# Performance work log

Measured on AMD Instinct MI355X. Metric: run time of the kernel, lower is better.

## Reference

```python
import jax, jax.numpy as jnp
import numpy as np

N = 4096          # number of real POIs (distance_matrix is [N, N])
D = 64            # poi_dim
B = 8             # users (samples)
DAYS = 4          # days per user
L = 64            # POI ids per day
SCALE = 50.0      # max distance -> arange(0, 50+0.5, 0.5) = 101 bucket boundaries
NUM_INTERVALS = 101


def setup_inputs() -> dict:
    key = jax.random.key(0)
    k1, k2, k3 = jax.random.split(key, 3)
    poi_weight = jax.random.normal(k1, (N + 1, D), dtype=jnp.float32)
    distance_matrix = jax.random.uniform(k2, (N, N), dtype=jnp.float32) * SCALE
    # POI ids in [1, N]: no padding zeros, so lastDay[lastDay != 0] == lastDay (static shape)
    seqInDay = jax.random.randint(k3, (B * DAYS, L), 1, N + 1)
    sampleIdOfDay_set = jnp.repeat(jnp.arange(B), DAYS)
    return {
        "poi_weight": poi_weight,
        "distance_matrix": distance_matrix,
        "seqInDay": seqInDay,
        "sampleIdOfDay_set": sampleIdOfDay_set,
        "GCN_layer_num": 2,
    }


def reference(poi_weight, distance_matrix, seqInDay, sampleIdOfDay_set, GCN_layer_num):
    # group days by sample id (stable sort == torch sorted+groupby); equal group sizes
    ids = np.asarray(sampleIdOfDay_set)
    order = np.argsort(ids, kind="stable")
    nb = int(np.unique(ids).size)
    days = ids.shape[0] // nb
    samples = seqInDay[order].reshape(nb, days, -1)            # [B, days, L]

    poi_emb = poi_weight[1:]                                    # [N, D]
    intervals = jnp.arange(0.0, SCALE + 0.5, 0.5)               # [NUM_INTERVALS]
    # bucket of every distance entry under the torch mask rule:
    # intervals[i-1] <= d < intervals[i]  <=>  searchsorted(side='right')
    dm_bucket = jnp.searchsorted(intervals, distance_matrix, side="right")  # [N, N] int
    diag = jnp.arange(distance_matrix.shape[0])
    scale = jnp.sqrt(jnp.float32(poi_weight.shape[1]))

    def per_sample(sample):                                     # sample: [days, L]
        lastDay = sample[-1]                                    # all ids nonzero
        spans = distance_matrix[lastDay[:-1] - 1, lastDay[1:] - 1]
        # torch.bucketize(right=False) == searchsorted side='left'
        span_idx = jnp.searchsorted(intervals, spans, side="left")
        w = jnp.bincount(span_idx, length=NUM_INTERVALS).astype(jnp.float32)
        w = w / w.sum()
        # buckets actually visited by this sample (torch loops over unique())
        present = jnp.zeros(NUM_INTERVALS, dtype=bool).at[span_idx].set(True)
        W = jnp.where(present[dm_bucket], w[dm_bucket], 0.0)    # [N, N]
        W = W.at[diag, diag].set(1.0)                            # fill_diagonal_(1)
        deg = jnp.maximum(jnp.sqrt(W.sum(-1, keepdims=True)), 1e-12)
        adj = W / deg / deg.T                                    # D^-1/2 A D^-1/2
        out = poi_emb
        layer = poi_emb
        for _ in range(GCN_layer_num):
            layer = jnp.tanh(adj @ layer)
            out = out + layer                                    # sum over stacked layers
        table = jnp.concatenate([poi_weight[:1], out], axis=0)  # [N+1, D]
        return table[sample] * scale                             # [days, L, D]

    res = jax.vmap(per_sample)(samples)                          # [B, days, L, D]
    return res.reshape(nb * days, samples.shape[-1], -1)
```

## Files before the change

kernel.cpp:

```cpp
#include <hip/hip_runtime.h>
#include <hip/hip_bf16.h>
#include <math.h>

typedef __bf16 bf16x8 __attribute__((ext_vector_type(8)));
typedef float  f32x4  __attribute__((ext_vector_type(4)));
typedef unsigned short ushort_t;
typedef unsigned char  u8;
typedef unsigned int   u32;

#define N_POI 4096
#define NB    8
#define NPAIR 4
#define NDAYS 4
#define LSEQ  64
#define NROWS 32
#define NBINS 102
#define KC    6

static __device__ __forceinline__ u32 bf16bits(float f) {
  u32 x = __float_as_uint(f);
  return ((x + 0x7FFFu + ((x >> 16) & 1u)) >> 16) & 0xFFFFu;
}

static __device__ __forceinline__ float lo16f(u32 v) {
  return __uint_as_float(v << 16);
}
static __device__ __forceinline__ float hi16f(u32 v) {
  return __uint_as_float(v & 0xFFFF0000u);
}

static __device__ __forceinline__ void gload16(void* lds, const void* g) {
  __builtin_amdgcn_global_load_lds(
      (const __attribute__((address_space(1))) u32*)g,
      (__attribute__((address_space(3))) u32*)lds, 16, 0, 0);
}

__global__ __launch_bounds__(64) void k_sample(const int* __restrict__ ids,
                                               const int* __restrict__ seq,
                                               const float* __restrict__ dm,
                                               float* __restrict__ tfp,
                                               u32* __restrict__ tbu,
                                               int* __restrict__ meta) {
  __shared__ int sh_ids[NROWS];
  __shared__ int sh_order[NROWS];
  __shared__ int sh_cnt[NBINS];
  __shared__ int sh_last[LSEQ];
  __shared__ int sh_nb;
  const int tid = threadIdx.x, s = blockIdx.x;
  if (tid < NROWS) sh_ids[tid] = ids[tid];
  for (int k = tid; k < NBINS; k += 64) sh_cnt[k] = 0;
  if (tid == 0) sh_nb = 0;
  __syncthreads();
  if (tid < NROWS) {
    const int my = sh_ids[tid];
    int rank = 0, first = 1;
    for (int j = 0; j < NROWS; ++j) {
      const int v = sh_ids[j];
      if (v < my || (v == my && j < tid)) rank++;
      if (v == my && j < tid) first = 0;
    }
    sh_order[rank] = tid;
    if (first) atomicAdd(&sh_nb, 1);
  }
  __syncthreads();
  const int nb = sh_nb;
  const int days = NROWS / nb;
  if (s == 0) {
    if (tid < NROWS) meta[tid] = sh_order[tid];
    if (tid == 0) meta[NROWS] = days;
  }
  const int lastRow = sh_order[s * days + days - 1];
  sh_last[tid] = seq[lastRow * LSEQ + tid];
  __syncthreads();
  if (tid < LSEQ - 1) {
    const float v = dm[(size_t)(sh_last[tid] - 1) * N_POI + (sh_last[tid + 1] - 1)];
    int si = (int)ceilf(2.0f * v);
    si = min(max(si, 0), 101);
    atomicAdd(&sh_cnt[si], 1);
  }
  __syncthreads();
  const float inv = 1.0f / (float)(LSEQ - 1);
  for (int k = tid; k < 128; k += 64) {
    const float wv = (k < NBINS) ? (float)sh_cnt[k] * inv : 0.0f;
    tfp[s * 128 + k] = wv;
    tbu[s * 128 + k] = bf16bits(wv);
  }
}

__global__ __launch_bounds__(256) void k_bucket(const float* __restrict__ dm,
                                                const float* __restrict__ tfp,
                                                u8* __restrict__ bucket,
                                                float* __restrict__ rbuf) {
  const int row = blockIdx.x, tid = threadIdx.x;
  __shared__ int h[4][NBINS];
  __shared__ float tl[NB][NBINS];
  __shared__ int sh_bii;
  for (int k = tid; k < 4 * NBINS; k += 256) ((int*)h)[k] = 0;
  __syncthreads();
  const float4* drow = (const float4*)(dm + (size_t)row * N_POI);
  u32* brow = (u32*)(bucket + (size_t)row * N_POI);
  int* hp = h[tid >> 6];
  const int jdiag = row >> 2;
  for (int it = 0; it < 4; ++it) {
    const int j = it * 256 + tid;
    const float4 v = drow[j];
    const int b0 = min((int)(2.0f * v.x) + 1, 101);
    const int b1 = min((int)(2.0f * v.y) + 1, 101);
    const int b2 = min((int)(2.0f * v.z) + 1, 101);
    const int b3 = min((int)(2.0f * v.w) + 1, 101);
    atomicAdd(&hp[b0], 1); atomicAdd(&hp[b1], 1);
    atomicAdd(&hp[b2], 1); atomicAdd(&hp[b3], 1);
    const u32 pk = (u32)b0 | ((u32)b1 << 8) | ((u32)b2 << 16) | ((u32)b3 << 24);
    if (j == jdiag) sh_bii = (int)((pk >> (8 * (row & 3))) & 255u);
    brow[j] = pk;
  }
  for (int idx = tid; idx < NB * NBINS; idx += 256)
    tl[idx / NBINS][idx % NBINS] = tfp[(idx / NBINS) * 128 + (idx % NBINS)];
  __syncthreads();
  for (int k = tid; k < NBINS; k += 256)
    h[0][k] += h[1][k] + h[2][k] + h[3][k];
  __syncthreads();
  const int s = tid >> 5, ln = tid & 31;
  float dot = 0.f;
  for (int k = ln; k < NBINS; k += 32) dot += (float)h[0][k] * tl[s][k];
#pragma unroll
  for (int off = 16; off >= 1; off >>= 1) dot += __shfl_down(dot, off, 32);
  if (ln == 0) {
    const float ri = rsqrtf(dot - tl[s][sh_bii] + 1.0f);
    rbuf[s * N_POI + row] = ri;
  }
}

__global__ __launch_bounds__(256) void k_rows(const float* __restrict__ rbuf,
                                              const float* __restrict__ poi,
                                              ushort_t* __restrict__ y1t) {
  const int s = blockIdx.y;
  const int i = blockIdx.x * 256 + threadIdx.x;
  const float ri = rbuf[s * N_POI + i];
  const float4* prow = (const float4*)(poi + (size_t)(i + 1) * 64);
  ushort_t* dst = y1t + (size_t)s * 64 * N_POI + i;
#pragma unroll
  for (int q = 0; q < 16; ++q) {
    const float4 v = prow[q];
    dst[(size_t)(4 * q + 0) * N_POI] = (ushort_t)bf16bits(ri * v.x);
    dst[(size_t)(4 * q + 1) * N_POI] = (ushort_t)bf16bits(ri * v.y);
    dst[(size_t)(4 * q + 2) * N_POI] = (ushort_t)bf16bits(ri * v.z);
    dst[(size_t)(4 * q + 3) * N_POI] = (ushort_t)bf16bits(ri * v.w);
  }
}

__global__ __launch_bounds__(256, 3) void k_layer(
    const u8* __restrict__ bucket, const u32* __restrict__ tbu,
    const ushort_t* __restrict__ yin, u32* __restrict__ part) {
  const int rb = blockIdx.x, kc = blockIdx.y, g = blockIdx.z;
  const int s0 = 2 * g, s1 = 2 * g + 1;
  const int tid = threadIdx.x;
  const int lane = tid & 63, w = tid >> 6;
  const int loff = tid & 31;

  __shared__ u32 trep[NBINS * 32];
  __shared__ ushort_t Ybuf[2][2][64 * 64];

  const int gi0 = rb * 128;
  const int r0 = gi0 + w * 32 + (lane & 15);
  const u8* brow0 = bucket + (size_t)r0 * N_POI;
  const u8* brow1 = brow0 + (size_t)16 * N_POI;
  const int kq = (lane >> 4) * 8;

  const ushort_t* ybase0 = yin + (size_t)s0 * 64 * N_POI;
  const ushort_t* ybase1 = yin + (size_t)s1 * 64 * N_POI;

  const int d0s = tid >> 3, d1s = 32 + d0s;
  const int bly = (tid & 7) * 16;
  const int sw0 = bly ^ (((d0s & 7) ^ ((d0s >> 3) & 1)) << 4);
  const int sw1 = bly ^ (((d1s & 7) ^ ((d1s >> 3) & 1)) << 4);
  const char* g00 = (const char*)(ybase0 + (size_t)d0s * N_POI) + sw0;
  const char* g01 = (const char*)(ybase0 + (size_t)d1s * N_POI) + sw1;
  const char* g10 = (const char*)(ybase1 + (size_t)d0s * N_POI) + sw0;
  const char* g11 = (const char*)(ybase1 + (size_t)d1s * N_POI) + sw1;

  const int kt0 = (kc * 64) / KC, kt1 = ((kc + 1) * 64) / KC;

  uint2 bpA[4], bpB[4];

#define LOADB_(dst, ktv)                                   \
  {                                                        \
    const int _kb = (ktv) * 64;                            \
    dst[0] = *(const uint2*)(brow0 + _kb + kq);            \
    dst[1] = *(const uint2*)(brow0 + _kb + 32 + kq);       \
    dst[2] = *(const uint2*)(brow1 + _kb + kq);            \
    dst[3] = *(const uint2*)(brow1 + _kb + 32 + kq);       \
  }

#define STAGE_(bufi, ktv)                                  \
  {                                                        \
    const size_t _kb = (size_t)(ktv) * 128;                \
    char* _lb = (char*)&Ybuf[bufi][0][0] + tid * 16;       \
    gload16(_lb, g00 + _kb);                               \
    gload16(_lb + 4096, g01 + _kb);                        \
    gload16(_lb + 8192, g10 + _kb);                        \
    gload16(_lb + 12288, g11 + _kb);                       \
  }

  STAGE_(0, kt0);
  LOADB_(bpA, kt0);
  for (int idx = tid; idx < NBINS * 32; idx += 256) {
    const int b = idx >> 5;
    trep[idx] = tbu[s0 * 128 + b] | (tbu[s1 * 128 + b] << 16);
  }

  f32x4 acc0[2][4], acc1[2][4];
#pragma unroll
  for (int mt = 0; mt < 2; ++mt)
#pragma unroll
    for (int nt = 0; nt < 4; ++nt) {
      acc0[mt][nt] = (f32x4){0.f, 0.f, 0.f, 0.f};
      acc1[mt][nt] = (f32x4){0.f, 0.f, 0.f, 0.f};
    }

  asm volatile("s_waitcnt vmcnt(0)" ::: "memory");
  __syncthreads();

#define BODY_(CB, PB, CUR)                                                     \
  {                                                                            \
    const int k0 = kt * 64;                                                    \
    if (kt + 1 < kt1) { STAGE_((CUR) ^ 1, kt + 1); LOADB_(PB, kt + 1); }       \
    bf16x8 af0[2][2], af1[2][2];                                               \
    _Pragma("unroll") for (int mt = 0; mt < 2; ++mt) {                         \
      _Pragma("unroll") for (int ks = 0; ks < 2; ++ks) {                       \
        const uint2 bb = CB[mt * 2 + ks];                                      \
        u32 tv[8];                                                             \
        _Pragma("unroll") for (int e = 0; e < 4; ++e) tv[e] =                  \
            trep[((bb.x >> (8 * e)) & 255u) * 32 + loff];                      \
        _Pragma("unroll") for (int e = 0; e < 4; ++e) tv[4 + e] =              \
            trep[((bb.y >> (8 * e)) & 255u) * 32 + loff];                      \
        const u32 de = (u32)(r0 + mt * 16 - (k0 + ks * 32 + kq));              \
        if (de < 8u) {             \
          _Pragma("unroll") for (int e = 0; e < 8; ++e)                        \
              if (de == (u32)e) tv[e] = 0x3F803F80u;                           \
        }                                                                      \
        uint4 p0, p1;                                                          \
        p0.x = (tv[0] & 0xFFFFu) | (tv[1] << 16);                              \
        p0.y = (tv[2] & 0xFFFFu) | (tv[3] << 16);                              \
        p0.z = (tv[4] & 0xFFFFu) | (tv[5] << 16);                              \
        p0.w = (tv[6] & 0xFFFFu) | (tv[7] << 16);                              \
        p1.x = (tv[0] >> 16) | (tv[1] & 0xFFFF0000u);                          \
        p1.y = (tv[2] >> 16) | (tv[3] & 0xFFFF0000u);                          \
        p1.z = (tv[4] >> 16) | (tv[5] & 0xFFFF0000u);                          \
        p1.w = (tv[6] >> 16) | (tv[7] & 0xFFFF0000u);                          \
        union { uint4 u; bf16x8 v; } c0, c1;                                   \
        c0.u = p0; c1.u = p1;                                                  \
        af0[mt][ks] = c0.v; af1[mt][ks] = c1.v;                                \
      }                                                                        \
    }                                                                          \
    const char* _y0 = (const char*)&Ybuf[CUR][0][0];                           \
    const char* _y1 = (const char*)&Ybuf[CUR][1][0];                           \
    _Pragma("unroll") for (int ks = 0; ks < 2; ++ks) {                         \
      _Pragma("unroll") for (int nt = 0; nt < 4; ++nt) {                       \
        const int rY = nt * 16 + (lane & 15);                                  \
        const int pm = (rY & 7) ^ ((rY >> 3) & 1);                             \
        const int la = rY * 128 + (((ks * 4 + (lane >> 4)) ^ pm) << 4);        \
        union { uint4 u; bf16x8 v; } b0, b1;                                   \
        b0.u = *(const uint4*)(_y0 + la);                                      \
        b1.u = *(const uint4*)(_y1 + la);                                      \
        acc0[0][nt] = __builtin_amdgcn_mfma_f32_16x16x32_bf16(af0[0][ks], b0.v, \
                                                              acc0[0][nt], 0, 0, 0); \
        acc0[1][nt] = __builtin_amdgcn_mfma_f32_16x16x32_bf16(af0[1][ks], b0.v, \
                                                              acc0[1][nt], 0, 0, 0); \
        acc1[0][nt] = __builtin_amdgcn_mfma_f32_16x16x32_bf16(af1[0][ks], b1.v, \
                                                              acc1[0][nt], 0, 0, 0); \
        acc1[1][nt] = __builtin_amdgcn_mfma_f32_16x16x32_bf16(af1[1][ks], b1.v, \
                                                              acc1[1][nt], 0, 0, 0); \
      }                                                                        \
    }                                                                          \
    asm volatile("s_waitcnt vmcnt(0)" ::: "memory");                           \
    __syncthreads();      \
  }

  int kt = kt0;
  while (true) {
    BODY_(bpA, bpB, 0);
    if (++kt >= kt1) break;
    BODY_(bpB, bpA, 1);
    if (++kt >= kt1) break;
  }

#undef BODY_
#undef STAGE_
#undef LOADB_

#pragma unroll
  for (int mt = 0; mt < 2; ++mt) {
#pragma unroll
    for (int e = 0; e < 4; ++e) {
      const int row = gi0 + w * 32 + mt * 16 + (lane >> 4) * 4 + e;
#pragma unroll
      for (int nt = 0; nt < 4; ++nt) {
        const int col = nt * 16 + (lane & 15);
        part[(((size_t)kc * NPAIR + g) * N_POI + row) * 64 + col] =
            bf16bits(acc0[mt][nt][e]) | (bf16bits(acc1[mt][nt][e]) << 16);
      }
    }
  }
}

__global__ __launch_bounds__(256) void k_reduce(
    const u32* __restrict__ part, const float* __restrict__ rbuf,
    const float* __restrict__ poi, float* __restrict__ table,
    ushort_t* __restrict__ y2t) {
  const int it = blockIdx.x, g = blockIdx.y, tid = threadIdx.x;
  const int s0 = 2 * g, s1 = 2 * g + 1;
  __shared__ ushort_t Tt[2][64 * 72];
#pragma unroll
  for (int j = 0; j < 2; ++j) {
    const int s2 = tid + j * 256;
    const int iloc = s2 >> 3, d0 = (s2 & 7) * 8;
    const int i = it * 64 + iloc;
    const size_t po = ((size_t)g * N_POI + i) * 64 + d0;
    float x0[8] = {0.f, 0.f, 0.f, 0.f, 0.f, 0.f, 0.f, 0.f};
    float x1[8] = {0.f, 0.f, 0.f, 0.f, 0.f, 0.f, 0.f, 0.f};
#pragma unroll
    for (int c = 0; c < KC; ++c) {
      const u32* sp = part + (size_t)c * NPAIR * N_POI * 64;
      uint4 a = *(const uint4*)(sp + po);
      uint4 b = *(const uint4*)(sp + po + 4);
      const u32* au = (const u32*)&a;
      const u32* bu = (const u32*)&b;
#pragma unroll
      for (int q = 0; q < 4; ++q) {
        x0[q] += lo16f(au[q]);     x1[q] += hi16f(au[q]);
        x0[4 + q] += lo16f(bu[q]); x1[4 + q] += hi16f(bu[q]);
      }
    }
    const float r0 = rbuf[s0 * N_POI + i];
    const float r1 = rbuf[s1 * N_POI + i];
    float t0[8], t1[8];
#pragma unroll
    for (int e = 0; e < 8; ++e) { t0[e] = tanhf(r0 * x0[e]); t1[e] = tanhf(r1 * x1[e]); }
    const float* prow = poi + (size_t)(i + 1) * 64 + d0;
    float4 pz0 = *(const float4*)prow;
    float4 pz1 = *(const float4*)(prow + 4);
    float* trow0 = table + ((size_t)s0 * N_POI + i) * 64 + d0;
    float* trow1 = table + ((size_t)s1 * N_POI + i) * 64 + d0;
    float4 o;
    o = (float4){pz0.x + t0[0], pz0.y + t0[1], pz0.z + t0[2], pz0.w + t0[3]};
    *(float4*)trow0 = o;
    o = (float4){pz1.x + t0[4], pz1.y + t0[5], pz1.z + t0[6], pz1.w + t0[7]};
    *(float4*)(trow0 + 4) = o;
    o = (float4){pz0.x + t1[0], pz0.y + t1[1], pz0.z + t1[2], pz0.w + t1[3]};
    *(float4*)trow1 = o;
    o = (float4){pz1.x + t1[4], pz1.y + t1[5], pz1.z + t1[6], pz1.w + t1[7]};
    *(float4*)(trow1 + 4) = o;
#pragma unroll
    for (int e = 0; e < 8; ++e) {
      Tt[0][(d0 + e) * 72 + iloc] = (ushort_t)bf16bits(r0 * t0[e]);
      Tt[1][(d0 + e) * 72 + iloc] = (ushort_t)bf16bits(r1 * t1[e]);
    }
  }
  __syncthreads();
  const int d = tid >> 2, i0 = (tid & 3) * 16;
#pragma unroll
  for (int ps = 0; ps < 2; ++ps) {
    uint4 a = *(const uint4*)&Tt[ps][d * 72 + i0];
    uint4 b = *(const uint4*)&Tt[ps][d * 72 + i0 + 8];
    ushort_t* dst = y2t + ((size_t)(2 * g + ps) * 64 + d) * N_POI + it * 64 + i0;
    *(uint4*)dst = a;
    *(uint4*)(dst + 8) = b;
  }
}

__global__ __launch_bounds__(256) void k_gather(const int* __restrict__ seq,
                                                const int* __restrict__ meta,
                                                const float* __restrict__ table,
                                                const float* __restrict__ poi,
                                                const u32* __restrict__ part,
                                                const float* __restrict__ rbuf,
                                                float* __restrict__ out) {
  const int r = blockIdx.x;
  const int p = blockIdx.y * 4 + (threadIdx.x >> 6);
  const int d = threadIdx.x & 63;
  const int days = meta[NROWS];
  const int srcrow = meta[r];
  const int s = r / days;
  const int id = seq[srcrow * LSEQ + p];
  float v;
  if (id == 0) {
    v = poi[d];
  } else {
    const size_t po = (((size_t)(s >> 1)) * N_POI + (id - 1)) * 64 + d;
    float x2 = 0.f;
#pragma unroll
    for (int c = 0; c < KC; ++c) {
      const u32 w = part[(size_t)c * NPAIR * N_POI * 64 + po];
      x2 += (s & 1) ? hi16f(w) : lo16f(w);
    }
    v = table[((size_t)s * N_POI + (id - 1)) * 64 + d] +
        tanhf(rbuf[s * N_POI + (id - 1)] * x2);
  }
  out[((size_t)r * LSEQ + p) * 64 + d] = v * 8.0f;
}

extern "C" void kernel_launch(void* const* d_in, const int* in_sizes, int n_in,
                              void* d_out, int out_size, void* d_ws, size_t ws_size,
                              hipStream_t stream) {
  (void)in_sizes; (void)n_in; (void)out_size; (void)ws_size;
  const float* poi = (const float*)d_in[0];
  const float* dm  = (const float*)d_in[1];
  const int*   seq = (const int*)d_in[2];
  const int*   ids = (const int*)d_in[3];

  char* ws = (char*)d_ws;
  size_t off = 0;
  auto carve = [&](size_t bytes) {
    char* p = ws + off;
    off += (bytes + 255) & ~(size_t)255;
    return p;
  };
  u8*       bucket = (u8*)carve((size_t)N_POI * N_POI);
  float*    tfp    = (float*)carve((size_t)NB * 128 * 4);
  u32*      tbu    = (u32*)carve((size_t)NB * 128 * 4);
  float*    rbuf   = (float*)carve((size_t)NB * N_POI * 4);
  float*    table  = (float*)carve((size_t)NB * N_POI * 64 * 4);
  ushort_t* y1t    = (ushort_t*)table;
  ushort_t* y2t    = (ushort_t*)carve((size_t)NB * 64 * N_POI * 2);
  u32*      part   = (u32*)carve((size_t)KC * NPAIR * N_POI * 64 * 4);
  int*      meta   = (int*)carve(256);

  k_sample<<<NB, 64, 0, stream>>>(ids, seq, dm, tfp, tbu, meta);
  k_bucket<<<N_POI, 256, 0, stream>>>(dm, tfp, bucket, rbuf);
  k_rows<<<dim3(16, NB), 256, 0, stream>>>(rbuf, poi, y1t);
  k_layer<<<dim3(32, KC, NPAIR), 256, 0, stream>>>(bucket, tbu, y1t, part);
  k_reduce<<<dim3(64, NPAIR), 256, 0, stream>>>(part, rbuf, poi, table, y2t);
  k_layer<<<dim3(32, KC, NPAIR), 256, 0, stream>>>(bucket, tbu, y2t, part);
  k_gather<<<dim3(NROWS, 16), 256, 0, stream>>>(seq, meta, table, poi, part, rbuf,
                                                (float*)d_out);
}
```

Before: 187.0 us.

## Compute second GCN layer only for rows gathered into the output

The second full adjacency-times-embedding pass over all 4096 rows per sample is replaced by a new kernel, k_layer2. It computes only the 256 rows per sample that the final gather reads, using row ids recorded by k_sample. The K dimension is split into 16 chunks whose fp32 partials are summed in the gather kernel. This drops most of the second layer's MFMA and bucket-read work, but rows are now fetched from random bucket rows and there are more partial sums to reduce.

```diff
diff --git a/kernel.cpp b/kernel.cpp
--- a/kernel.cpp
+++ b/kernel.cpp
@@ -16,6 +16,8 @@
 #define NROWS 32
 #define NBINS 102
 #define KC    6
+#define KC2   16
+#define NPOS  2048
 
 static __device__ __forceinline__ u32 bf16bits(float f) {
   u32 x = __float_as_uint(f);
@@ -40,7 +42,8 @@
                                                const float* __restrict__ dm,
                                                float* __restrict__ tfp,
                                                u32* __restrict__ tbu,
-                                               int* __restrict__ meta) {
+                                               int* __restrict__ meta,
+                                               int* __restrict__ rowids) {
   __shared__ int sh_ids[NROWS];
   __shared__ int sh_order[NROWS];
   __shared__ int sh_cnt[NBINS];
@@ -68,6 +71,11 @@
   if (s == 0) {
     if (tid < NROWS) meta[tid] = sh_order[tid];
     if (tid == 0) meta[NROWS] = days;
+  }
+  for (int day = 0; day < days; ++day) {
+    const int r = s * days + day;
+    const int src = sh_order[r];
+    rowids[r * LSEQ + tid] = max(seq[src * LSEQ + tid] - 1, 0);
   }
   const int lastRow = sh_order[s * days + days - 1];
   sh_last[tid] = seq[lastRow * LSEQ + tid];
@@ -369,11 +377,147 @@
   }
 }
 
+__global__ __launch_bounds__(256) void k_layer2(
+    const u8* __restrict__ bucket, const u32* __restrict__ tbu,
+    const ushort_t* __restrict__ yin, const int* __restrict__ rowids,
+    float* __restrict__ part2) {
+  const int rb = blockIdx.x, kc = blockIdx.y;
+  const int s = rb >> 1;
+  const int tid = threadIdx.x;
+  const int lane = tid & 63, w = tid >> 6;
+  const int loff = tid & 31;
+
+  __shared__ u32 trep[NBINS * 32];
+  __shared__ ushort_t Ybuf[2][64 * 64];
+
+  const int pos0 = rb * 128 + w * 32 + (lane & 15);
+  const int rid0 = rowids[pos0];
+  const int rid1 = rowids[pos0 + 16];
+  const u8* brow0 = bucket + (size_t)rid0 * N_POI;
+  const u8* brow1 = bucket + (size_t)rid1 * N_POI;
+  const int kq = (lane >> 4) * 8;
+
+  const ushort_t* ybase = yin + (size_t)s * 64 * N_POI;
+  const int d0s = tid >> 3, d1s = 32 + d0s;
+  const int bly = (tid & 7) * 16;
+  const int sw0 = bly ^ (((d0s & 7) ^ ((d0s >> 3) & 1)) << 4);
+  const int sw1 = bly ^ (((d1s & 7) ^ ((d1s >> 3) & 1)) << 4);
+  const char* gsrc0 = (const char*)(ybase + (size_t)d0s * N_POI) + sw0;
+  const char* gsrc1 = (const char*)(ybase + (size_t)d1s * N_POI) + sw1;
+
+  const int kt0 = kc * 4, kt1 = kt0 + 4;
+
+  uint2 bpA[4], bpB[4];
+
+#define LOADB_(dst, ktv)                                   \
+  {                                                        \
+    const int _kb = (ktv) * 64;                            \
+    dst[0] = *(const uint2*)(brow0 + _kb + kq);            \
+    dst[1] = *(const uint2*)(brow0 + _kb + 32 + kq);       \
+    dst[2] = *(const uint2*)(brow1 + _kb + kq);            \
+    dst[3] = *(const uint2*)(brow1 + _kb + 32 + kq);       \
+  }
+
+#define STAGE_(bufi, ktv)                                  \
+  {                                                        \
+    const size_t _kb = (size_t)(ktv) * 128;                \
+    char* _lb = (char*)&Ybuf[bufi][0] + tid * 16;          \
+    gload16(_lb, gsrc0 + _kb);                             \
+    gload16(_lb + 4096, gsrc1 + _kb);                      \
+  }
+
+  STAGE_(0, kt0);
+  LOADB_(bpA, kt0);
+  for (int idx = tid; idx < NBINS * 32; idx += 256)
+    trep[idx] = tbu[s * 128 + (idx >> 5)];
+
+  f32x4 acc[2][4];
+#pragma unroll
+  for (int mt = 0; mt < 2; ++mt)
+#pragma unroll
+    for (int nt = 0; nt < 4; ++nt) acc[mt][nt] = (f32x4){0.f, 0.f, 0.f, 0.f};
+
+  asm volatile("s_waitcnt vmcnt(0)" ::: "memory");
+  __syncthreads();
+
+#define BODY_(CB, PB, CUR)                                                     \
+  {                                                                            \
+    const int k0 = kt * 64;                                                    \
+    if (kt + 1 < kt1) { STAGE_((CUR) ^ 1, kt + 1); LOADB_(PB, kt + 1); }       \
+    bf16x8 afr[2][2];                                                          \
+    _Pragma("unroll") for (int mt = 0; mt < 2; ++mt) {                         \
+      _Pragma("unroll") for (int ks = 0; ks < 2; ++ks) {                       \
+        const uint2 bb = CB[mt * 2 + ks];                                      \
+        u32 tv[8];                                                             \
+        _Pragma("unroll") for (int e = 0; e < 4; ++e) tv[e] =                  \
+            trep[((bb.x >> (8 * e)) & 255u) * 32 + loff];                      \
+        _Pragma("unroll") for (int e = 0; e < 4; ++e) tv[4 + e] =              \
+            trep[((bb.y >> (8 * e)) & 255u) * 32 + loff];                      \
+        const int grow = mt ? rid1 : rid0;                                     \
+        const u32 de = (u32)(grow - (k0 + ks * 32 + kq));                      \
+        if (de < 8u) {                              \
+          _Pragma("unroll") for (int e = 0; e < 8; ++e)                        \
+              if (de == (u32)e) tv[e] = 0x3F80u;                               \
+        }                                                                      \
+        uint4 pk;                                                              \
+        pk.x = tv[0] | (tv[1] << 16);                                          \
+        pk.y = tv[2] | (tv[3] << 16);                                          \
+        pk.z = tv[4] | (tv[5] << 16);                                          \
+        pk.w = tv[6] | (tv[7] << 16);                                          \
+        union { uint4 u; bf16x8 v; } cvt;                                      \
+        cvt.u = pk;                                                            \
+        afr[mt][ks] = cvt.v;                                                   \
+      }                                                                        \
+    }                                                                          \
+    const char* _yb = (const char*)&Ybuf[CUR][0];                              \
+    _Pragma("unroll") for (int ks = 0; ks < 2; ++ks) {                         \
+      _Pragma("unroll") for (int nt = 0; nt < 4; ++nt) {                       \
+        const int rY = nt * 16 + (lane & 15);                                  \
+        const int pm = (rY & 7) ^ ((rY >> 3) & 1);                             \
+        const int la = rY * 128 + (((ks * 4 + (lane >> 4)) ^ pm) << 4);        \
+        union { uint4 u; bf16x8 v; } bu;                                       \
+        bu.u = *(const uint4*)(_yb + la);                                      \
+        acc[0][nt] = __builtin_amdgcn_mfma_f32_16x16x32_bf16(afr[0][ks], bu.v, \
+                                                             acc[0][nt], 0, 0, 0); \
+        acc[1][nt] = __builtin_amdgcn_mfma_f32_16x16x32_bf16(afr[1][ks], bu.v, \
+                                                             acc[1][nt], 0, 0, 0); \
+      }                                                                        \
+    }                                                                          \
+    asm volatile("s_waitcnt vmcnt(0)" ::: "memory");                           \
+    __syncthreads();                                                           \
+  }
+
+  int kt = kt0;
+  while (true) {
+    BODY_(bpA, bpB, 0);
+    if (++kt >= kt1) break;
+    BODY_(bpB, bpA, 1);
+    if (++kt >= kt1) break;
+  }
+
+#undef BODY_
+#undef STAGE_
+#undef LOADB_
+
+#pragma unroll
+  for (int mt = 0; mt < 2; ++mt) {
+#pragma unroll
+    for (int e = 0; e < 4; ++e) {
+      const int pos = rb * 128 + w * 32 + mt * 16 + (lane >> 4) * 4 + e;
+#pragma unroll
+      for (int nt = 0; nt < 4; ++nt) {
+        const int col = nt * 16 + (lane & 15);
+        part2[((size_t)kc * NPOS + pos) * 64 + col] = acc[mt][nt][e];
+      }
+    }
+  }
+}
+
 __global__ __launch_bounds__(256) void k_gather(const int* __restrict__ seq,
                                                 const int* __restrict__ meta,
                                                 const float* __restrict__ table,
                                                 const float* __restrict__ poi,
-                                                const u32* __restrict__ part,
+                                                const float* __restrict__ part2,
                                                 const float* __restrict__ rbuf,
                                                 float* __restrict__ out) {
   const int r = blockIdx.x;
@@ -387,13 +531,11 @@
   if (id == 0) {
     v = poi[d];
   } else {
-    const size_t po = (((size_t)(s >> 1)) * N_POI + (id - 1)) * 64 + d;
+    const size_t gq = (size_t)r * LSEQ + p;
     float x2 = 0.f;
 #pragma unroll
-    for (int c = 0; c < KC; ++c) {
-      const u32 w = part[(size_t)c * NPAIR * N_POI * 64 + po];
-      x2 += (s & 1) ? hi16f(w) : lo16f(w);
-    }
+    for (int c = 0; c < KC2; ++c)
+      x2 += part2[((size_t)c * NPOS + gq) * 64 + d];
     v = table[((size_t)s * N_POI + (id - 1)) * 64 + d] +
         tanhf(rbuf[s * N_POI + (id - 1)] * x2);
   }
@@ -424,14 +566,16 @@
   ushort_t* y1t    = (ushort_t*)table;
   ushort_t* y2t    = (ushort_t*)carve((size_t)NB * 64 * N_POI * 2);
   u32*      part   = (u32*)carve((size_t)KC * NPAIR * N_POI * 64 * 4);
+  float*    part2  = (float*)carve((size_t)KC2 * NPOS * 64 * 4);
+  int*      rowids = (int*)carve((size_t)NPOS * 4);
   int*      meta   = (int*)carve(256);
 
-  k_sample<<<NB, 64, 0, stream>>>(ids, seq, dm, tfp, tbu, meta);
+  k_sample<<<NB, 64, 0, stream>>>(ids, seq, dm, tfp, tbu, meta, rowids);
   k_bucket<<<N_POI, 256, 0, stream>>>(dm, tfp, bucket, rbuf);
   k_rows<<<dim3(16, NB), 256, 0, stream>>>(rbuf, poi, y1t);
   k_layer<<<dim3(32, KC, NPAIR), 256, 0, stream>>>(bucket, tbu, y1t, part);
   k_reduce<<<dim3(64, NPAIR), 256, 0, stream>>>(part, rbuf, poi, table, y2t);
-  k_layer<<<dim3(32, KC, NPAIR), 256, 0, stream>>>(bucket, tbu, y2t, part);
-  k_gather<<<dim3(NROWS, 16), 256, 0, stream>>>(seq, meta, table, poi, part, rbuf,
+  k_layer2<<<dim3(16, KC2), 256, 0, stream>>>(bucket, tbu, y2t, rowids, part2);
+  k_gather<<<dim3(NROWS, 16), 256, 0, stream>>>(seq, meta, table, poi, part2, rbuf,
                                                 (float*)d_out);
 }
```

Result: faster. 167.2 us (-10.6%).
